# Performance work log

Hardware: AMD Instinct MI355X
Metric: run time of the kernel (lower is better)

Reference implementation:

```python
import jax, jax.numpy as jnp
import numpy as np

DIM = 1024
N_HEADS = 16
HEAD_DIM = DIM // N_HEADS  # 64
FF_DIM = 4096
BATCH = 2
SEQ = 2048
EPS = 1e-8
ROPE_BASE = 10000.0


def _rope_cos_sin(seq_len, head_dim):
    # inv_freq: [head_dim//2]
    inv_freq = 1.0 / (ROPE_BASE ** (jnp.arange(0, head_dim, 2, dtype=jnp.float32) / head_dim))
    t = jnp.arange(seq_len, dtype=jnp.float32)
    freqs = jnp.einsum('i,j->ij', t, inv_freq)          # [S, D/2]
    emb = jnp.concatenate([freqs, freqs], axis=-1)       # [S, D]
    return jnp.cos(emb), jnp.sin(emb)


def _apply_rope(x, cos, sin):
    # x: [B, S, H, D]; cos/sin: [S, D] -> broadcast [1, S, 1, D]
    d2 = x.shape[-1] // 2
    x1, x2 = x[..., :d2], x[..., d2:]
    cos = cos[None, :, None, :]
    sin = sin[None, :, None, :]
    cos1, cos2 = cos[..., :d2], cos[..., d2:]
    sin1, sin2 = sin[..., :d2], sin[..., d2:]
    return jnp.concatenate([x1 * cos1 - x2 * sin1, x1 * sin2 + x2 * cos2], axis=-1)


def _rmsnorm(x, scale):
    # norm = ||x||_2 * d^{-1/2}; out = scale * x / (norm + eps)
    norm = jnp.sqrt(jnp.sum(x * x, axis=-1, keepdims=True)) * (x.shape[-1] ** -0.5)
    return scale * x / (norm + EPS)


def setup_inputs() -> dict:
    key = jax.random.key(0)
    ks = jax.random.split(key, 10)
    s = lambda fan_in: 1.0 / np.sqrt(fan_in)
    return {
        'x': jax.random.normal(ks[0], (BATCH, SEQ, DIM), dtype=jnp.float32),
        'w_qkv': jax.random.normal(ks[1], (DIM, 3 * DIM), dtype=jnp.float32) * s(DIM),
        'w_attn_out': jax.random.normal(ks[2], (DIM, DIM), dtype=jnp.float32) * s(DIM),
        'w_gate': jax.random.normal(ks[3], (DIM, FF_DIM), dtype=jnp.float32) * s(DIM),
        'b_gate': jax.random.normal(ks[4], (FF_DIM,), dtype=jnp.float32) * 0.01,
        'w_lin': jax.random.normal(ks[5], (DIM, FF_DIM), dtype=jnp.float32) * s(DIM),
        'b_lin': jax.random.normal(ks[6], (FF_DIM,), dtype=jnp.float32) * 0.01,
        'w_ff_out': jax.random.normal(ks[7], (FF_DIM, DIM), dtype=jnp.float32) * s(FF_DIM),
        'scale1': jnp.ones((DIM,), dtype=jnp.float32),
        'scale2': jnp.ones((DIM,), dtype=jnp.float32),
    }


def reference(x, w_qkv, w_attn_out, w_gate, b_gate, w_lin, b_lin, w_ff_out, scale1, scale2):
    B, S, _ = x.shape
    residual = x
    qkv = (x @ w_qkv).reshape(B, S, 3, N_HEADS, HEAD_DIM)
    q, k, v = qkv[:, :, 0], qkv[:, :, 1], qkv[:, :, 2]  # [B, S, H, D]
    cos, sin = _rope_cos_sin(S, HEAD_DIM)
    q = _apply_rope(q, cos, sin)
    k = _apply_rope(k, cos, sin)
    # attention scores [B, H, S, S]
    attn = jnp.einsum('bqhd,bkhd->bhqk', q, k) / np.sqrt(HEAD_DIM).astype(np.float32)
    attn = jax.nn.softmax(attn, axis=-1)
    out = jnp.einsum('bhqk,bkhd->bqhd', attn, v).reshape(B, S, DIM)
    out = out @ w_attn_out
    x = _rmsnorm(residual + out, scale1)
    residual = x
    ff = jax.nn.sigmoid(x @ w_gate + b_gate) * (x @ w_lin + b_lin)
    ff = ff @ w_ff_out
    x = _rmsnorm(residual + ff, scale2)
    return x
```

## Files before the change

### kernel.cpp

```cpp
#include <hip/hip_runtime.h>
#include <stdint.h>

#define DIMN 1024
#define NH 16
#define HD 64
#define FFN 4096
#define BBATCH 2
#define SSEQ 2048
#define MROWS (BBATCH*SSEQ)

typedef __bf16 bf16;
typedef __bf16 bf16x8 __attribute__((ext_vector_type(8)));
typedef __bf16 bf16x4 __attribute__((ext_vector_type(4)));
typedef float f32x4 __attribute__((ext_vector_type(4)));
typedef float f32x16 __attribute__((ext_vector_type(16)));
typedef uint32_t u32x4 __attribute__((ext_vector_type(4)));

#define AS1 __attribute__((address_space(1)))
#define AS3 __attribute__((address_space(3)))

__device__ __forceinline__ void gload16(const bf16* g, bf16* l) {
  __builtin_amdgcn_global_load_lds((AS1 const void*)g, (AS3 void*)l, 16, 0, 0);
}

__device__ __forceinline__ uint32_t pkbf(float a, float b) {
  union { bf16 h[2]; uint32_t u; } x;
  x.h[0] = (bf16)a; x.h[1] = (bf16)b;
  return x.u;
}

__global__ void rope_table_kernel(float* __restrict__ tab) {
  int i = blockIdx.x * blockDim.x + threadIdx.x;
  int s = i >> 5, d = i & 31;
  float invf = exp2f(-(float)d * 0.4152410118609203f);
  float fr = (float)s * invf;
  tab[s*64 + d]      = cosf(fr);
  tab[s*64 + 32 + d] = sinf(fr);
}

__global__ void cast_f32_bf16(const float* __restrict__ in, bf16* __restrict__ out, int n4) {
  int i = blockIdx.x * blockDim.x + threadIdx.x;
  if (i < n4) {
    f32x4 v = ((const f32x4*)in)[i];
    bf16x4 o = {(bf16)v.x, (bf16)v.y, (bf16)v.z, (bf16)v.w};
    ((bf16x4*)out)[i] = o;
  }
}

__global__ __launch_bounds__(256) void transpose_cast_f32_bf16(
    const float* __restrict__ in, bf16* __restrict__ out, int R, int C) {
  __shared__ float t[32][33];
  int bx = blockIdx.x, by = blockIdx.y;
  int x = threadIdx.x, y = threadIdx.y;
  #pragma unroll
  for (int j = 0; j < 4; ++j) {
    int r = by*32 + y*4 + j;
    t[y*4+j][x] = in[(size_t)r*C + bx*32 + x];
  }
  __syncthreads();
  #pragma unroll
  for (int j = 0; j < 4; ++j) {
    int c = bx*32 + y*4 + j;
    out[(size_t)c*R + by*32 + x] = (bf16)t[x][y*4+j];
  }
}

template<int NP>
__global__ __launch_bounds__(256) void rmsnorm_sum_kernel(
    const float* __restrict__ parts, const float* __restrict__ resid,
    const float* __restrict__ sc,
    float* __restrict__ outf, bf16* __restrict__ outb) {
  int row = blockIdx.x;
  int tid = threadIdx.x;
  size_t off = (size_t)row * DIMN;
  f32x4 v = ((const f32x4*)(resid + off))[tid];
  #pragma unroll
  for (int p = 0; p < NP; ++p) {
    f32x4 a = ((const f32x4*)(parts + (size_t)p * MROWS * DIMN + off))[tid];
    v.x += a.x; v.y += a.y; v.z += a.z; v.w += a.w;
  }
  float ss = v.x*v.x + v.y*v.y + v.z*v.z + v.w*v.w;
  #pragma unroll
  for (int m = 1; m < 64; m <<= 1) ss += __shfl_xor(ss, m);
  __shared__ float red[4];
  if ((tid & 63) == 0) red[tid >> 6] = ss;
  __syncthreads();
  float tot = red[0] + red[1] + red[2] + red[3];
  float inv = 1.f / (sqrtf(tot) * 0.03125f + 1e-8f);
  f32x4 s4 = ((const f32x4*)sc)[tid];
  f32x4 o = {v.x*s4.x*inv, v.y*s4.y*inv, v.z*s4.z*inv, v.w*s4.w*inv};
  if (outf) ((f32x4*)(outf + off))[tid] = o;
  if (outb) {
    bf16x4 ob = {(bf16)o.x, (bf16)o.y, (bf16)o.z, (bf16)o.w};
    ((bf16x4*)(outb + off))[tid] = ob;
  }
}

template<int EPI>
__global__ void __launch_bounds__(256, 2) gemm_bt(
    const bf16* __restrict__ A, const bf16* __restrict__ B,
    int M, int N, int K,
    void* __restrict__ o0, void* __restrict__ o1, void* __restrict__ o2,
    const void* __restrict__ a0, const void* __restrict__ a1) {
  __shared__ __align__(16) bf16 sh_a[2*4096];
  __shared__ __align__(16) bf16 sh_b[2*4096];
  const int tid  = threadIdx.x;
  const int lane = tid & 63;
  const int wid  = tid >> 6;

  int gx  = gridDim.x;
  int bid = blockIdx.y * gx + blockIdx.x;
  int nwg = gx * gridDim.y;
  int cpx = nwg >> 3;
  int swz = (bid & 7) * cpx + (bid >> 3);
  int bxi = swz % gx, byi = swz / gx;

  const int m0 = byi * 128, n0 = bxi * 128;
  const int wm = (wid >> 1) * 64, wn = (wid & 1) * 64;

  const int kb = blockIdx.z;
  const int KC = K / (int)gridDim.z;

  f32x4 acc[4][4] = {};

  const bf16* a_base = A + (size_t)m0 * K + (size_t)kb * KC;
  const bf16* b_base = B + (size_t)n0 * K + (size_t)kb * KC;

  auto stage = [&](int kt, int buf) {
    const int lb = buf * 4096;
    #pragma unroll
    for (int i = 0; i < 2; ++i) {
      int idx = i*256 + tid;
      size_t go = (size_t)(idx >> 2)*K + (size_t)kt*32 + (idx & 3)*8;
      gload16(a_base + go, &sh_a[lb + idx*8]);
    }
    #pragma unroll
    for (int i = 0; i < 2; ++i) {
      int idx = i*256 + tid;
      size_t go = (size_t)(idx >> 2)*K + (size_t)kt*32 + (idx & 3)*8;
      gload16(b_base + go, &sh_b[lb + idx*8]);
    }
  };

  const int nsteps = KC >> 5;
  stage(0, 0);
  for (int t = 0; t < nsteps; ++t) {
    const int cb = t & 1;
    if (t + 1 < nsteps) {
      stage(t+1, cb ^ 1);
      asm volatile("s_waitcnt vmcnt(4)" ::: "memory");
    } else {
      asm volatile("s_waitcnt vmcnt(0)" ::: "memory");
    }
    __builtin_amdgcn_sched_barrier(0);
    __builtin_amdgcn_s_barrier();
    __builtin_amdgcn_sched_barrier(0);

    const int lb = cb * 4096;
    bf16x8 af[4], bfr[4];
    #pragma unroll
    for (int m = 0; m < 4; ++m)
      af[m] = *(const bf16x8*)&sh_a[lb + (wm + m*16 + (lane & 15))*32 + (lane >> 4)*8];
    #pragma unroll
    for (int n = 0; n < 4; ++n)
      bfr[n] = *(const bf16x8*)&sh_b[lb + (wn + n*16 + (lane & 15))*32 + (lane >> 4)*8];
    __builtin_amdgcn_s_setprio(1);
    #pragma unroll
    for (int m = 0; m < 4; ++m)
      #pragma unroll
      for (int n = 0; n < 4; ++n)
        acc[m][n] = __builtin_amdgcn_mfma_f32_16x16x32_bf16(af[m], bfr[n], acc[m][n], 0, 0, 0);
    __builtin_amdgcn_s_setprio(0);
    __builtin_amdgcn_sched_barrier(0);
    __builtin_amdgcn_s_barrier();
  }

  const int rq = (lane >> 4) * 4;
  const int cl = lane & 15;

  if constexpr (EPI == 0) {
    bf16* q_p = (bf16*)o0; bf16* k_p = (bf16*)o1; bf16* v_p = (bf16*)o2;
    const float* rope = (const float*)a0;
    int sec = (n0 + wn) >> 10;
    int h   = ((n0 + wn) & 1023) >> 6;
    const float qsc = (sec == 0) ? 0.18033688011112042f : 1.0f;
    #pragma unroll
    for (int m = 0; m < 4; ++m) {
      #pragma unroll
      for (int reg = 0; reg < 4; ++reg) {
        int r  = m0 + wm + m*16 + rq + reg;
        int b_ = r >> 11, s_ = r & 2047;
        int tile = s_ >> 5;
        size_t tb = ((size_t)(b_*NH + h) * 64 + tile) * 2048;
        if (sec == 2) {
          int kvl = s_ & 31;
          int ks = kvl >> 4, hiv = (kvl >> 3) & 1, jv = kvl & 7;
          #pragma unroll
          for (int n = 0; n < 4; ++n) {
            int half = n >> 1;
            int qlv  = (n & 1) * 16 + cl;
            v_p[tb + (size_t)(ks*2 + half)*512 + (hiv*32 + qlv)*8 + jv] =
                (bf16)acc[m][n][reg];
          }
        } else {
          int qlt = s_ & 31;
          bf16* dst = (sec == 0 ? q_p : k_p);
          int lo = ((cl >> 3) * 32 + qlt) * 8 + (cl & 7);
          #pragma unroll
          for (int n = 0; n < 2; ++n) {
            int d1 = n*16 + cl;
            float c1 = rope[s_*64 + d1];
            float s1 = rope[s_*64 + 32 + d1];
            float x1 = acc[m][n][reg], x2 = acc[m][n+2][reg];
            dst[tb + (size_t)n*512 + lo]       = (bf16)((x1*c1 - x2*s1) * qsc);
            dst[tb + (size_t)(n+2)*512 + lo]   = (bf16)((x1*s1 + x2*c1) * qsc);
          }
        }
      }
    }
  } else if constexpr (EPI == 4) {
    float* op = (float*)o0 + (size_t)kb * M * N;
    #pragma unroll
    for (int m = 0; m < 4; ++m)
      #pragma unroll
      for (int n = 0; n < 4; ++n)
        #pragma unroll
        for (int reg = 0; reg < 4; ++reg) {
          int r = m0 + wm + m*16 + rq + reg;
          int c = n0 + wn + n*16 + cl;
          op[(size_t)r*N + c] = acc[m][n][reg];
        }
  }
}

__global__ void __launch_bounds__(512, 2) gemm256_ffn1(
    const bf16* __restrict__ A, const bf16* __restrict__ Bg,
    const bf16* __restrict__ Bl, int M, int N, int K,
    bf16* __restrict__ o0, const float* __restrict__ bgv,
    const float* __restrict__ blv) {
  __shared__ __align__(16) bf16 shA[4][256*32];
  const int tid  = threadIdx.x;
  const int lane = tid & 63;
  const int wid  = tid >> 6;
  const int wr   = wid >> 2;
  const int wc   = wid & 3;

  int gx  = gridDim.x;
  int bid = blockIdx.y * gx + blockIdx.x;
  int nwg = gx * gridDim.y;
  int cpx = nwg >> 3;
  int swz = (bid & 7) * cpx + (bid >> 3);
  int bxi = swz % gx, byi = swz / gx;
  const int m0 = byi * 256, n0 = bxi * 128;

  const int nt = K >> 5;

  const bf16* a_base  = A  + (size_t)m0 * K;
  const bf16* bg_base = Bg + (size_t)(n0 + wc*32) * K;
  const bf16* bl_base = Bl + (size_t)(n0 + wc*32) * K;

  const int fr = lane & 15, fq = lane >> 4;

  const int srow = tid >> 2;
  const int snom = tid & 3;
  const int sgl  = snom ^ (srow & 3);
  auto stA = [&](int kt, int s) {
    #pragma unroll
    for (int c = 0; c < 2; ++c) {
      int row = c*128 + srow;
      gload16(a_base + (size_t)row*K + (size_t)kt*32 + sgl*8,
              &shA[s][row*32 + snom*8]);
    }
  };
  auto ldBC = [&](int kt, bf16x8* bb, bf16x8* cc) {
    #pragma unroll
    for (int n = 0; n < 2; ++n) {
      bb[n] = *(const bf16x8*)(bg_base + (size_t)(n*16 + fr)*K + (size_t)kt*32 + fq*8);
      cc[n] = *(const bf16x8*)(bl_base + (size_t)(n*16 + fr)*K + (size_t)kt*32 + fq*8);
    }
  };

  f32x4 acc [8][2] = {};
  f32x4 acc2[8][2] = {};
  bf16x8 bcur[2], ccur[2], bnxt[2], cnxt[2];

  stA(0, 0); stA(1, 1); stA(2, 2);
  ldBC(0, bcur, ccur);

  const int aslot = (fq ^ (fr & 3)) * 8;

  for (int t = 0; t < nt; ++t) {
    const int s = t & 3;
    if (t + 3 < nt) stA(t+3, (t+3) & 3);
    if (t + 1 < nt) ldBC(t+1, bnxt, cnxt);
    if (t + 3 < nt)      asm volatile("s_waitcnt vmcnt(10)" ::: "memory");
    else if (t + 1 < nt) asm volatile("s_waitcnt vmcnt(8)" ::: "memory");
    else                 asm volatile("s_waitcnt vmcnt(0)" ::: "memory");
    __builtin_amdgcn_sched_barrier(0);
    __builtin_amdgcn_s_barrier();
    __builtin_amdgcn_sched_barrier(0);

    {
      bf16x8 af[4];
      #pragma unroll
      for (int m = 0; m < 4; ++m)
        af[m] = *(const bf16x8*)&shA[s][(wr*128 + m*16 + fr)*32 + aslot];
      __builtin_amdgcn_s_setprio(1);
      #pragma unroll
      for (int m = 0; m < 4; ++m)
        #pragma unroll
        for (int n = 0; n < 2; ++n) {
          acc [m][n] = __builtin_amdgcn_mfma_f32_16x16x32_bf16(af[m], bcur[n], acc [m][n], 0, 0, 0);
          acc2[m][n] = __builtin_amdgcn_mfma_f32_16x16x32_bf16(af[m], ccur[n], acc2[m][n], 0, 0, 0);
        }
      __builtin_amdgcn_s_setprio(0);
    }
    {
      bf16x8 af[4];
      #pragma unroll
      for (int m = 0; m < 4; ++m)
        af[m] = *(const bf16x8*)&shA[s][(wr*128 + (m+4)*16 + fr)*32 + aslot];
      __builtin_amdgcn_s_setprio(1);
      #pragma unroll
      for (int m = 0; m < 4; ++m)
        #pragma unroll
        for (int n = 0; n < 2; ++n) {
          acc [m+4][n] = __builtin_amdgcn_mfma_f32_16x16x32_bf16(af[m], bcur[n], acc [m+4][n], 0, 0, 0);
          acc2[m+4][n] = __builtin_amdgcn_mfma_f32_16x16x32_bf16(af[m], ccur[n], acc2[m+4][n], 0, 0, 0);
        }
      __builtin_amdgcn_s_setprio(0);
    }
    __builtin_amdgcn_sched_barrier(0);
    __builtin_amdgcn_s_barrier();
    #pragma unroll
    for (int n = 0; n < 2; ++n) { bcur[n] = bnxt[n]; ccur[n] = cnxt[n]; }
  }

  const int rq = (lane >> 4) * 4;
  const int cl = lane & 15;
  #pragma unroll
  for (int m = 0; m < 8; ++m)
    #pragma unroll
    for (int n = 0; n < 2; ++n)
      #pragma unroll
      for (int reg = 0; reg < 4; ++reg) {
        int r = m0 + wr*128 + m*16 + rq + reg;
        int c = n0 + wc*32 + n*16 + cl;
        float gv = acc [m][n][reg] + bgv[c];
        float lv = acc2[m][n][reg] + blv[c];
        float sg = 1.f / (1.f + __expf(-gv));
        o0[(size_t)r*N + c] = (bf16)(sg * lv);
      }
}

__global__ void __launch_bounds__(256) attn_kernel(
    const bf16* __restrict__ qf_g, const bf16* __restrict__ kf_g,
    const bf16* __restrict__ vf_g, bf16* __restrict__ ao_g) {
  __shared__ __align__(16) bf16 lds_k[2*2048];
  __shared__ __align__(16) bf16 lds_v[2*2048];
  const int tid  = threadIdx.x;
  const int lane = tid & 63;
  const int qw   = tid >> 6;
  const int hi   = lane >> 5;
  const int ql   = lane & 31;
  const int bh   = blockIdx.y;
  const int b_   = bh >> 4, h = bh & 15;
  const int q0   = blockIdx.x * 128 + qw * 32;
  const int qt   = blockIdx.x * 4 + qw;

  const bf16* qtile = qf_g + ((size_t)bh*64 + qt) * 2048;
  const bf16* kbase = kf_g + (size_t)bh * 64 * 2048;
  const bf16* vbase = vf_g + (size_t)bh * 64 * 2048;

  bf16x8 qf[4];
  #pragma unroll
  for (int ds = 0; ds < 4; ++ds)
    qf[ds] = *(const bf16x8*)&qtile[ds*512 + lane*8];

  f32x16 o0 = {}, o1 = {};
  float lrun = 0.f;

  gload16(kbase + tid*8, &lds_k[tid*8]);
  gload16(vbase + tid*8, &lds_v[tid*8]);

  for (int t = 0; t < 64; ++t) {
    const int cur = (t & 1) * 2048;
    if (t < 63) {
      const int nxt = 2048 - cur;
      gload16(kbase + (size_t)(t+1)*2048 + tid*8, &lds_k[nxt + tid*8]);
      gload16(vbase + (size_t)(t+1)*2048 + tid*8, &lds_v[nxt + tid*8]);
      asm volatile("s_waitcnt vmcnt(2)" ::: "memory");
    } else {
      asm volatile("s_waitcnt vmcnt(0)" ::: "memory");
    }
    __builtin_amdgcn_sched_barrier(0);
    __builtin_amdgcn_s_barrier();
    __builtin_amdgcn_sched_barrier(0);

    f32x16 st = {};
    __builtin_amdgcn_s_setprio(1);
    #pragma unroll
    for (int ds = 0; ds < 4; ++ds) {
      bf16x8 kf = *(const bf16x8*)&lds_k[cur + ds*512 + lane*8];
      st = __builtin_amdgcn_mfma_f32_32x32x16_bf16(kf, qf[ds], st, 0, 0, 0);
    }
    __builtin_amdgcn_s_setprio(0);
    float p[16];
    float psum = 0.f;
    #pragma unroll
    for (int r = 0; r < 16; ++r) { p[r] = __builtin_amdgcn_exp2f(st[r]); psum += p[r]; }
    lrun += psum;

    uint32_t w0 = pkbf(p[0],p[1]),   w1 = pkbf(p[2],p[3]);
    uint32_t w2 = pkbf(p[4],p[5]),   w3 = pkbf(p[6],p[7]);
    uint32_t w4 = pkbf(p[8],p[9]),   w5 = pkbf(p[10],p[11]);
    uint32_t w6 = pkbf(p[12],p[13]), w7 = pkbf(p[14],p[15]);
    asm("v_permlane32_swap_b32 %0, %1" : "+v"(w0), "+v"(w2));
    asm("v_permlane32_swap_b32 %0, %1" : "+v"(w1), "+v"(w3));
    asm("v_permlane32_swap_b32 %0, %1" : "+v"(w4), "+v"(w6));
    asm("v_permlane32_swap_b32 %0, %1" : "+v"(w5), "+v"(w7));

    __builtin_amdgcn_s_setprio(1);
    {
      union { u32x4 u; bf16x8 b; } pu;
      u32x4 pwa = {w0, w1, w2, w3};
      pu.u = pwa;
      bf16x8 v0 = *(const bf16x8*)&lds_v[cur + 0*512 + lane*8];
      bf16x8 v1 = *(const bf16x8*)&lds_v[cur + 1*512 + lane*8];
      o0 = __builtin_amdgcn_mfma_f32_32x32x16_bf16(v0, pu.b, o0, 0, 0, 0);
      o1 = __builtin_amdgcn_mfma_f32_32x32x16_bf16(v1, pu.b, o1, 0, 0, 0);
      u32x4 pwb = {w4, w5, w6, w7};
      pu.u = pwb;
      bf16x8 v2 = *(const bf16x8*)&lds_v[cur + 2*512 + lane*8];
      bf16x8 v3 = *(const bf16x8*)&lds_v[cur + 3*512 + lane*8];
      o0 = __builtin_amdgcn_mfma_f32_32x32x16_bf16(v2, pu.b, o0, 0, 0, 0);
      o1 = __builtin_amdgcn_mfma_f32_32x32x16_bf16(v3, pu.b, o1, 0, 0, 0);
    }
    __builtin_amdgcn_s_setprio(0);

    __builtin_amdgcn_sched_barrier(0);
    __builtin_amdgcn_s_barrier();
    __builtin_amdgcn_sched_barrier(0);
  }

  lrun += __shfl_xor(lrun, 32);
  float inv = 1.f / lrun;
  bf16* aop = ao_g + ((size_t)(b_*SSEQ) + q0 + ql) * DIMN + h*HD;
  #pragma unroll
  for (int g = 0; g < 4; ++g) {
    int dbase = 8*g + 4*hi;
    bf16x4 w0 = {(bf16)(o0[4*g]*inv), (bf16)(o0[4*g+1]*inv),
                 (bf16)(o0[4*g+2]*inv), (bf16)(o0[4*g+3]*inv)};
    *(bf16x4*)&aop[dbase] = w0;
    bf16x4 w1 = {(bf16)(o1[4*g]*inv), (bf16)(o1[4*g+1]*inv),
                 (bf16)(o1[4*g+2]*inv), (bf16)(o1[4*g+3]*inv)};
    *(bf16x4*)&aop[32 + dbase] = w1;
  }
}

extern "C" void kernel_launch(void* const* d_in, const int* in_sizes, int n_in,
                              void* d_out, int out_size, void* d_ws, size_t ws_size,
                              hipStream_t stream) {
  const float* x      = (const float*)d_in[0];
  const float* w_qkv  = (const float*)d_in[1];
  const float* w_ao   = (const float*)d_in[2];
  const float* w_gate = (const float*)d_in[3];
  const float* b_gate = (const float*)d_in[4];
  const float* w_lin  = (const float*)d_in[5];
  const float* b_lin  = (const float*)d_in[6];
  const float* w_ffo  = (const float*)d_in[7];
  const float* scale1 = (const float*)d_in[8];
  const float* scale2 = (const float*)d_in[9];
  float* out = (float*)d_out;
  (void)ws_size; (void)in_sizes; (void)n_in; (void)out_size;

  uint8_t* ws = (uint8_t*)d_ws;
  bf16*  wt_ws   = (bf16*) (ws + 0);
  float* rope_ws = (float*)(ws + 8388608);
  bf16*  xb_ws   = (bf16*) (ws + 8912896);
  bf16*  ao_ws   = (bf16*) (ws + 8912896);
  bf16*  q_ws    = (bf16*) (ws + 17301504);
  bf16*  k_ws    = (bf16*) (ws + 25690112);
  bf16*  v_ws    = (bf16*) (ws + 34078720);
  float* p1_ws   = (float*)(ws + 17301504);
  bf16*  wt2_ws  = (bf16*) (ws + 50855936);
  bf16*  h1b_ws  = (bf16*) (ws + 84410368);
  bf16*  ffb_ws  = (bf16*) (ws + 8912896);
  float* p2_ws   = (float*)(ws + 42467328);
  float* h1f_ws  = (float*)(ws + 109576192);

  rope_table_kernel<<<256, 256, 0, stream>>>(rope_ws);
  cast_f32_bf16<<<4096, 256, 0, stream>>>(x, xb_ws, MROWS*DIMN/4);
  transpose_cast_f32_bf16<<<dim3(3*DIMN/32, DIMN/32), dim3(32,8), 0, stream>>>(w_qkv, wt_ws, DIMN, 3*DIMN);
  gemm_bt<0><<<dim3(24, 32), 256, 0, stream>>>(xb_ws, wt_ws, MROWS, 3*DIMN, DIMN,
                                               q_ws, k_ws, v_ws, rope_ws, nullptr);
  attn_kernel<<<dim3(16, 32), 256, 0, stream>>>(q_ws, k_ws, v_ws, ao_ws);
  transpose_cast_f32_bf16<<<dim3(DIMN/32, DIMN/32), dim3(32,8), 0, stream>>>(w_ao, wt_ws, DIMN, DIMN);
  gemm_bt<4><<<dim3(8, 32, 2), 256, 0, stream>>>(ao_ws, wt_ws, MROWS, DIMN, DIMN,
                                                 p1_ws, nullptr, nullptr, nullptr, nullptr);
  rmsnorm_sum_kernel<2><<<MROWS, 256, 0, stream>>>(p1_ws, x, scale1, h1f_ws, h1b_ws);
  transpose_cast_f32_bf16<<<dim3(FFN/32, DIMN/32), dim3(32,8), 0, stream>>>(w_gate, wt_ws, DIMN, FFN);
  transpose_cast_f32_bf16<<<dim3(FFN/32, DIMN/32), dim3(32,8), 0, stream>>>(w_lin, wt2_ws, DIMN, FFN);
  gemm256_ffn1<<<dim3(32, 16), 512, 0, stream>>>(h1b_ws, wt_ws, wt2_ws, MROWS, FFN, DIMN,
                                                 ffb_ws, b_gate, b_lin);
  transpose_cast_f32_bf16<<<dim3(DIMN/32, FFN/32), dim3(32,8), 0, stream>>>(w_ffo, wt_ws, FFN, DIMN);
  gemm_bt<4><<<dim3(8, 32, 4), 256, 0, stream>>>(ffb_ws, wt_ws, MROWS, DIMN, FFN,
                                                 p2_ws, nullptr, nullptr, nullptr, nullptr);
  rmsnorm_sum_kernel<4><<<MROWS, 256, 0, stream>>>(p2_ws, h1f_ws, scale2, out, nullptr);
}
```

Measured before the change: 348.6 us.

## Pre-pack FFN1 weights into MFMA fragment order and retile gate/lin GEMM

Replaces the transpose-cast of w_gate and w_lin with a kernel that casts and packs them directly into per-lane MFMA fragment order, so the GEMM loads each B fragment with one coalesced 16-byte read. The fused gate/linear GEMM goes from 256x128 tiles with 512 threads and 4-stage A buffering to 128x128 tiles with 256 threads, 4x4 fragments per wave and a double-buffered A. The A tile drops its XOR swizzle, which may cause LDS bank conflicts. The packing kernel reads the fp32 weights with strided, uncoalesced accesses, which may cost more than the transpose it replaces.

```diff
diff --git a/kernel.cpp b/kernel.cpp
--- a/kernel.cpp
+++ b/kernel.cpp
@@ -63,6 +63,22 @@
     int c = bx*32 + y*4 + j;
     out[(size_t)c*R + by*32 + x] = (bf16)t[x][y*4+j];
   }
+}
+
+__global__ __launch_bounds__(256) void pack_wfrag(
+    const float* __restrict__ W, bf16* __restrict__ WF, int K, int N) {
+  int g = blockIdx.x * 4 + (threadIdx.x >> 6);
+  int l = threadIdx.x & 63;
+  int KT = K >> 5;
+  int n  = g & 3;
+  int kt = (g >> 2) % KT;
+  int cb = (g >> 2) / KT;
+  int c  = cb*64 + n*16 + (l & 15);
+  int k0 = kt*32 + (l >> 4)*8;
+  bf16x8 v;
+  #pragma unroll
+  for (int j = 0; j < 8; ++j) v[j] = (bf16)W[(size_t)(k0 + j)*N + c];
+  *(bf16x8*)&WF[((size_t)g*64 + l)*8] = v;
 }
 
 template<int NP>
@@ -233,17 +249,15 @@
   }
 }
 
-__global__ void __launch_bounds__(512, 2) gemm256_ffn1(
-    const bf16* __restrict__ A, const bf16* __restrict__ Bg,
-    const bf16* __restrict__ Bl, int M, int N, int K,
+__global__ void __launch_bounds__(256, 2) gemm_ffn1_rw(
+    const bf16* __restrict__ A, const bf16* __restrict__ WgF,
+    const bf16* __restrict__ WlF, int M, int N, int K,
     bf16* __restrict__ o0, const float* __restrict__ bgv,
     const float* __restrict__ blv) {
-  __shared__ __align__(16) bf16 shA[4][256*32];
+  __shared__ __align__(16) bf16 sh_a[2*4096];
   const int tid  = threadIdx.x;
   const int lane = tid & 63;
   const int wid  = tid >> 6;
-  const int wr   = wid >> 2;
-  const int wc   = wid & 3;
 
   int gx  = gridDim.x;
   int bid = blockIdx.y * gx + blockIdx.x;
@@ -251,101 +265,82 @@
   int cpx = nwg >> 3;
   int swz = (bid & 7) * cpx + (bid >> 3);
   int bxi = swz % gx, byi = swz / gx;
-  const int m0 = byi * 256, n0 = bxi * 128;
-
-  const int nt = K >> 5;
-
-  const bf16* a_base  = A  + (size_t)m0 * K;
-  const bf16* bg_base = Bg + (size_t)(n0 + wc*32) * K;
-  const bf16* bl_base = Bl + (size_t)(n0 + wc*32) * K;
-
-  const int fr = lane & 15, fq = lane >> 4;
-
-  const int srow = tid >> 2;
-  const int snom = tid & 3;
-  const int sgl  = snom ^ (srow & 3);
-  auto stA = [&](int kt, int s) {
-    #pragma unroll
-    for (int c = 0; c < 2; ++c) {
-      int row = c*128 + srow;
-      gload16(a_base + (size_t)row*K + (size_t)kt*32 + sgl*8,
-              &shA[s][row*32 + snom*8]);
+
+  const int m0 = byi * 128, n0 = bxi * 128;
+  const int wm = (wid >> 1) * 64, wn = (wid & 1) * 64;
+
+  const int KT = K >> 5;
+  const int wcb = (n0 + wn) >> 6;
+  const bf16* wg = WgF + (size_t)wcb * KT * 2048;
+  const bf16* wl = WlF + (size_t)wcb * KT * 2048;
+  const bf16* a_base = A + (size_t)m0 * K;
+
+  auto stageA = [&](int kt, int buf) {
+    #pragma unroll
+    for (int i = 0; i < 2; ++i) {
+      int idx = i*256 + tid;
+      size_t go = (size_t)(idx >> 2)*K + (size_t)kt*32 + (idx & 3)*8;
+      gload16(a_base + go, &sh_a[buf*4096 + idx*8]);
     }
   };
-  auto ldBC = [&](int kt, bf16x8* bb, bf16x8* cc) {
-    #pragma unroll
-    for (int n = 0; n < 2; ++n) {
-      bb[n] = *(const bf16x8*)(bg_base + (size_t)(n*16 + fr)*K + (size_t)kt*32 + fq*8);
-      cc[n] = *(const bf16x8*)(bl_base + (size_t)(n*16 + fr)*K + (size_t)kt*32 + fq*8);
+  auto ldW = [&](int kt, bf16x8* bb, bf16x8* cc) {
+    #pragma unroll
+    for (int n = 0; n < 4; ++n) {
+      bb[n] = *(const bf16x8*)&wg[(size_t)kt*2048 + n*512 + lane*8];
+      cc[n] = *(const bf16x8*)&wl[(size_t)kt*2048 + n*512 + lane*8];
     }
   };
 
-  f32x4 acc [8][2] = {};
-  f32x4 acc2[8][2] = {};
-  bf16x8 bcur[2], ccur[2], bnxt[2], cnxt[2];
-
-  stA(0, 0); stA(1, 1); stA(2, 2);
-  ldBC(0, bcur, ccur);
-
-  const int aslot = (fq ^ (fr & 3)) * 8;
-
-  for (int t = 0; t < nt; ++t) {
-    const int s = t & 3;
-    if (t + 3 < nt) stA(t+3, (t+3) & 3);
-    if (t + 1 < nt) ldBC(t+1, bnxt, cnxt);
-    if (t + 3 < nt)      asm volatile("s_waitcnt vmcnt(10)" ::: "memory");
-    else if (t + 1 < nt) asm volatile("s_waitcnt vmcnt(8)" ::: "memory");
-    else                 asm volatile("s_waitcnt vmcnt(0)" ::: "memory");
+  f32x4 acc[4][4] = {}, acc2[4][4] = {};
+  bf16x8 bcur[4], ccur[4], bnxt[4], cnxt[4];
+
+  ldW(0, bcur, ccur);
+  stageA(0, 0);
+  for (int t = 0; t < KT; ++t) {
+    const int cb = t & 1;
+    if (t + 1 < KT) {
+      ldW(t+1, bnxt, cnxt);
+      stageA(t+1, cb ^ 1);
+      asm volatile("s_waitcnt vmcnt(10)" ::: "memory");
+    } else {
+      asm volatile("s_waitcnt vmcnt(0)" ::: "memory");
+    }
     __builtin_amdgcn_sched_barrier(0);
     __builtin_amdgcn_s_barrier();
     __builtin_amdgcn_sched_barrier(0);
 
-    {
-      bf16x8 af[4];
+    const int lb = cb * 4096;
+    bf16x8 af[4];
+    #pragma unroll
+    for (int m = 0; m < 4; ++m)
+      af[m] = *(const bf16x8*)&sh_a[lb + (wm + m*16 + (lane & 15))*32 + (lane >> 4)*8];
+    __builtin_amdgcn_s_setprio(1);
+    #pragma unroll
+    for (int m = 0; m < 4; ++m)
       #pragma unroll
-      for (int m = 0; m < 4; ++m)
-        af[m] = *(const bf16x8*)&shA[s][(wr*128 + m*16 + fr)*32 + aslot];
-      __builtin_amdgcn_s_setprio(1);
+      for (int n = 0; n < 4; ++n) {
+        acc [m][n] = __builtin_amdgcn_mfma_f32_16x16x32_bf16(af[m], bcur[n], acc [m][n], 0, 0, 0);
+        acc2[m][n] = __builtin_amdgcn_mfma_f32_16x16x32_bf16(af[m], ccur[n], acc2[m][n], 0, 0, 0);
+      }
+    __builtin_amdgcn_s_setprio(0);
+    __builtin_amdgcn_sched_barrier(0);
+    __builtin_amdgcn_s_barrier();
+    if (t + 1 < KT) {
       #pragma unroll
-      for (int m = 0; m < 4; ++m)
-        #pragma unroll
-        for (int n = 0; n < 2; ++n) {
-          acc [m][n] = __builtin_amdgcn_mfma_f32_16x16x32_bf16(af[m], bcur[n], acc [m][n], 0, 0, 0);
-          acc2[m][n] = __builtin_amdgcn_mfma_f32_16x16x32_bf16(af[m], ccur[n], acc2[m][n], 0, 0, 0);
-        }
-      __builtin_amdgcn_s_setprio(0);
-    }
-    {
-      bf16x8 af[4];
-      #pragma unroll
-      for (int m = 0; m < 4; ++m)
-        af[m] = *(const bf16x8*)&shA[s][(wr*128 + (m+4)*16 + fr)*32 + aslot];
-      __builtin_amdgcn_s_setprio(1);
-      #pragma unroll
-      for (int m = 0; m < 4; ++m)
-        #pragma unroll
-        for (int n = 0; n < 2; ++n) {
-          acc [m+4][n] = __builtin_amdgcn_mfma_f32_16x16x32_bf16(af[m], bcur[n], acc [m+4][n], 0, 0, 0);
-          acc2[m+4][n] = __builtin_amdgcn_mfma_f32_16x16x32_bf16(af[m], ccur[n], acc2[m+4][n], 0, 0, 0);
-        }
-      __builtin_amdgcn_s_setprio(0);
-    }
-    __builtin_amdgcn_sched_barrier(0);
-    __builtin_amdgcn_s_barrier();
-    #pragma unroll
-    for (int n = 0; n < 2; ++n) { bcur[n] = bnxt[n]; ccur[n] = cnxt[n]; }
+      for (int n = 0; n < 4; ++n) { bcur[n] = bnxt[n]; ccur[n] = cnxt[n]; }
+    }
   }
 
   const int rq = (lane >> 4) * 4;
   const int cl = lane & 15;
   #pragma unroll
-  for (int m = 0; m < 8; ++m)
-    #pragma unroll
-    for (int n = 0; n < 2; ++n)
+  for (int m = 0; m < 4; ++m)
+    #pragma unroll
+    for (int n = 0; n < 4; ++n)
       #pragma unroll
       for (int reg = 0; reg < 4; ++reg) {
-        int r = m0 + wr*128 + m*16 + rq + reg;
-        int c = n0 + wc*32 + n*16 + cl;
+        int r = m0 + wm + m*16 + rq + reg;
+        int c = n0 + wn + n*16 + cl;
         float gv = acc [m][n][reg] + bgv[c];
         float lv = acc2[m][n][reg] + blv[c];
         float sg = 1.f / (1.f + __expf(-gv));
@@ -499,9 +494,9 @@
   gemm_bt<4><<<dim3(8, 32, 2), 256, 0, stream>>>(ao_ws, wt_ws, MROWS, DIMN, DIMN,
                                                  p1_ws, nullptr, nullptr, nullptr, nullptr);
   rmsnorm_sum_kernel<2><<<MROWS, 256, 0, stream>>>(p1_ws, x, scale1, h1f_ws, h1b_ws);
-  transpose_cast_f32_bf16<<<dim3(FFN/32, DIMN/32), dim3(32,8), 0, stream>>>(w_gate, wt_ws, DIMN, FFN);
-  transpose_cast_f32_bf16<<<dim3(FFN/32, DIMN/32), dim3(32,8), 0, stream>>>(w_lin, wt2_ws, DIMN, FFN);
-  gemm256_ffn1<<<dim3(32, 16), 512, 0, stream>>>(h1b_ws, wt_ws, wt2_ws, MROWS, FFN, DIMN,
+  pack_wfrag<<<2048, 256, 0, stream>>>(w_gate, wt_ws, DIMN, FFN);
+  pack_wfrag<<<2048, 256, 0, stream>>>(w_lin, wt2_ws, DIMN, FFN);
+  gemm_ffn1_rw<<<dim3(32, 32), 256, 0, stream>>>(h1b_ws, wt_ws, wt2_ws, MROWS, FFN, DIMN,
                                                  ffb_ws, b_gate, b_lin);
   transpose_cast_f32_bf16<<<dim3(DIMN/32, FFN/32), dim3(32,8), 0, stream>>>(w_ffo, wt_ws, FFN, DIMN);
   gemm_bt<4><<<dim3(8, 32, 4), 256, 0, stream>>>(ffb_ws, wt_ws, MROWS, DIMN, FFN,
```

New measurement: 308.7 us. 11.4% less time.
